# Kernel optimization log

Measured on AMD Instinct MI355X. Metric: run time of the kernel, lower is better.

Reference implementation:

```python
import jax, jax.numpy as jnp
import numpy as np

N, E, IN_F, H, F = 4096, 131072, 512, 8, 32  # n_nodes, n_edges, in_features, n_heads, n_hidden
SLOPE = 0.2


def setup_inputs() -> dict:
    key = jax.random.key(0)
    k1, k2, k3, k4 = jax.random.split(key, 4)
    h = jax.random.normal(k1, (N, IN_F), dtype=jnp.float32)
    edge_index = jax.random.randint(k2, (2, E), 0, N)
    train_mask = jnp.ones((E + N,), dtype=jnp.float32)  # mask values written into adj (incl. self-loops appended in forward)
    W_fc = jax.random.normal(k3, (IN_F, H * F), dtype=jnp.float32) * (1.0 / np.sqrt(IN_F))
    W_attn = jax.random.normal(k4, (2 * F,), dtype=jnp.float32) * (1.0 / np.sqrt(2 * F))
    return {"h": h, "edge_index": edge_index, "train_mask": train_mask, "W_fc": W_fc, "W_attn": W_attn}


def reference(h, edge_index, train_mask, W_fc, W_attn):
    n = h.shape[0]
    g = (h @ W_fc).reshape(n, H, F)  # [n, H, F]
    # attn_fc(concat(g_i, g_j)) == g_i @ W_attn[:F] + g_j @ W_attn[F:]  (same math, no NxNx2F tensor)
    el = g @ W_attn[:F]  # [n, H], contribution of source row i
    er = g @ W_attn[F:]  # [n, H], contribution of column j
    e = jax.nn.leaky_relu(el[:, None, :] + er[None, :, :], SLOPE)  # [n, n, H]
    # adjacency: edges (+ self-loops appended in forward) get train_mask values, then diagonal forced to 1
    src = jnp.concatenate([edge_index[0], jnp.arange(n)])
    dst = jnp.concatenate([edge_index[1], jnp.arange(n)])
    adj = jnp.zeros((n, n), dtype=h.dtype).at[src, dst].set(train_mask)
    diag = jnp.arange(n)
    adj = adj.at[diag, diag].set(1.0)
    e = jnp.where(adj[:, :, None] == 0, -jnp.inf, e)
    a = jax.nn.softmax(e, axis=1)  # softmax over neighbors j (dropout p=0 -> identity)
    attn_res = jnp.einsum('ijh,jhf->ihf', a, g)  # [n, H, F]
    return attn_res.reshape(n, H * F)  # is_concat=True
```

## Files before the change

kernel.cpp:

```cpp
#include <hip/hip_runtime.h>
#include <stdint.h>

#define NN   4096
#define NE   131072
#define KIN  512
#define NH   8
#define HF   256
#define SLOPE 0.2f
#define MAXJ 256

typedef __attribute__((ext_vector_type(8))) short bf16x8;
typedef __attribute__((ext_vector_type(4))) float f32x4;


__device__ __forceinline__ unsigned short f2bf(float x) {
  unsigned u = __builtin_bit_cast(unsigned, x);
  u += 0x7FFFu + ((u >> 16) & 1u);
  return (unsigned short)(u >> 16);
}
__device__ __forceinline__ float bf2f(unsigned short x) {
  unsigned u = ((unsigned)x) << 16;
  return __builtin_bit_cast(float, u);
}
__device__ __forceinline__ unsigned pack2(float lo, float hi) {
  return (unsigned)f2bf(lo) | ((unsigned)f2bf(hi) << 16);
}

__global__ __launch_bounds__(256) void prep_k(const float* __restrict__ B,
                                              unsigned* __restrict__ bitmap,
                                              unsigned short* __restrict__ Btbf) {
  __shared__ float tile[32][33];
  const int b = blockIdx.x, t = threadIdx.x;
  if (b < 128) {
    float4* p = (float4*)bitmap + (size_t)b * 1024;
#pragma unroll
    for (int it = 0; it < 4; ++it)
      p[it * 256 + t] = make_float4(0.f, 0.f, 0.f, 0.f);
  } else {
    int bb = b - 128;
    int k0 = (bb >> 3) * 32, n0 = (bb & 7) * 32;
    int lr = t >> 3, lc = (t & 7) * 4;
    float4 v = *(const float4*)&B[(size_t)(k0 + lr) * HF + n0 + lc];
    tile[lr][lc] = v.x; tile[lr][lc + 1] = v.y; tile[lr][lc + 2] = v.z; tile[lr][lc + 3] = v.w;
    __syncthreads();
    ushort4 o;
    o.x = f2bf(tile[lc + 0][lr]); o.y = f2bf(tile[lc + 1][lr]);
    o.z = f2bf(tile[lc + 2][lr]); o.w = f2bf(tile[lc + 3][lr]);
    *(ushort4*)&Btbf[(size_t)(n0 + lr) * KIN + k0 + lc] = o;
  }
}

__global__ __launch_bounds__(256) void gemm_adj_k(const float* __restrict__ h,
                                                  const unsigned short* __restrict__ Bt,
                                                  const float* __restrict__ Wa,
                                                  unsigned short* __restrict__ gbf,
                                                  float* __restrict__ el,
                                                  float* __restrict__ er,
                                                  const int* __restrict__ ei,
                                                  const float* __restrict__ mask,
                                                  unsigned* __restrict__ bitmap) {
  __shared__ unsigned short smem[2][6144];
  const int bx = blockIdx.x, t = threadIdx.x;
  if (bx >= 512) {
    int k = (bx - 512) * 256 + t;
    int s, d; float m;
    if (k < NE) { s = ei[k]; d = ei[NE + k]; m = mask[k]; }
    else        { s = k - NE; d = s; m = 1.0f; }
    if (m != 0.0f) atomicOr(&bitmap[s * 128 + (d >> 5)], 1u << (d & 31));
    return;
  }
  const int gx = bx & 127, gy = bx >> 7;
  const int row0 = gx * 32, col0 = gy * 64;
  const int w = t >> 6, l = t & 63;
  const int wr = w >> 1, wc = w & 1;

  const int srow = t >> 3;
  const int sc   = l & 7;
  const int aoff = srow * 64 + (((t & 7) ^ (srow & 7)) << 3);
  const float* gA = &h[(size_t)(row0 + srow) * KIN + (t & 7) * 8];
  const int bsrow = (w << 3) + (l >> 3);
  const int schB  = sc ^ (bsrow & 7);
  const unsigned short* gB0 = &Bt[(size_t)(col0 + bsrow) * KIN + schB * 8];
  const unsigned short* gB1 = &Bt[(size_t)(col0 + 32 + bsrow) * KIN + schB * 8];

#define BSTAGE(bf, ks)                                                                            \
  do {                                                                                            \
    __builtin_amdgcn_global_load_lds(                                                             \
        (const __attribute__((address_space(1))) unsigned int*)(gB0 + (size_t)(ks) * 64),         \
        (__attribute__((address_space(3))) unsigned int*)(&smem[bf][2048 + w * 512]), 16, 0, 0);  \
    __builtin_amdgcn_global_load_lds(                                                             \
        (const __attribute__((address_space(1))) unsigned int*)(gB1 + (size_t)(ks) * 64),         \
        (__attribute__((address_space(3))) unsigned int*)(&smem[bf][4096 + w * 512]), 16, 0, 0);  \
  } while (0)

  f32x4 acc0 = {}, acc1 = {};
  {
    float4 va0 = *(const float4*)(gA);
    float4 va1 = *(const float4*)(gA + 4);
    BSTAGE(0, 0);
    uint4 w4 = {pack2(va0.x, va0.y), pack2(va0.z, va0.w),
                pack2(va1.x, va1.y), pack2(va1.z, va1.w)};
    *(uint4*)&smem[0][aoff] = w4;
  }
  __syncthreads();

  const int lrow = l & 15, kg = l >> 4;
  const int ar  = wr * 16 + lrow;
  const int br0 = wc * 32 + lrow, br1 = wc * 32 + 16 + lrow;
  for (int ks = 0; ks < 8; ++ks) {
    const int bf = ks & 1;
    float4 na0, na1;
    if (ks < 7) {
      na0 = *(const float4*)(gA + (ks + 1) * 64);
      na1 = *(const float4*)(gA + (ks + 1) * 64 + 4);
      BSTAGE(bf ^ 1, ks + 1);
    }
    bf16x8 a0 = *(const bf16x8*)&smem[bf][ar * 64 + ((kg ^ (ar & 7)) << 3)];
    bf16x8 a1 = *(const bf16x8*)&smem[bf][ar * 64 + (((4 + kg) ^ (ar & 7)) << 3)];
    bf16x8 b00 = *(const bf16x8*)&smem[bf][2048 + br0 * 64 + ((kg ^ (br0 & 7)) << 3)];
    bf16x8 b01 = *(const bf16x8*)&smem[bf][2048 + br0 * 64 + (((4 + kg) ^ (br0 & 7)) << 3)];
    bf16x8 b10 = *(const bf16x8*)&smem[bf][2048 + br1 * 64 + ((kg ^ (br1 & 7)) << 3)];
    bf16x8 b11 = *(const bf16x8*)&smem[bf][2048 + br1 * 64 + (((4 + kg) ^ (br1 & 7)) << 3)];
    acc0 = __builtin_amdgcn_mfma_f32_16x16x32_bf16(a0, b00, acc0, 0, 0, 0);
    acc0 = __builtin_amdgcn_mfma_f32_16x16x32_bf16(a1, b01, acc0, 0, 0, 0);
    acc1 = __builtin_amdgcn_mfma_f32_16x16x32_bf16(a0, b10, acc1, 0, 0, 0);
    acc1 = __builtin_amdgcn_mfma_f32_16x16x32_bf16(a1, b11, acc1, 0, 0, 0);
    if (ks < 7) {
      uint4 w4 = {pack2(na0.x, na0.y), pack2(na0.z, na0.w),
                  pack2(na1.x, na1.y), pack2(na1.z, na1.w)};
      *(uint4*)&smem[bf ^ 1][aoff] = w4;
    }
    __syncthreads();
  }
#undef BSTAGE

  const int crow = (l >> 4) * 4, ccol = l & 15;
  const int gr0 = row0 + wr * 16 + crow;
  const int gc0 = col0 + wc * 32 + ccol, gc1 = gc0 + 16;
#pragma unroll
  for (int q = 0; q < 4; ++q) {
    gbf[(size_t)(gr0 + q) * HF + gc0] = f2bf(acc0[q]);
    gbf[(size_t)(gr0 + q) * HF + gc1] = f2bf(acc1[q]);
  }

  const int head = (gy << 1) + wc;
  const float wal0 = Wa[ccol],      wal1 = Wa[16 + ccol];
  const float war0 = Wa[32 + ccol], war1 = Wa[48 + ccol];
#pragma unroll
  for (int q = 0; q < 4; ++q) {
    float pel = acc0[q] * wal0 + acc1[q] * wal1;
    float per = acc0[q] * war0 + acc1[q] * war1;
#pragma unroll
    for (int m = 8; m >= 1; m >>= 1) { pel += __shfl_xor(pel, m); per += __shfl_xor(per, m); }
    if (ccol == 0) {
      el[(gr0 + q) * NH + head] = pel;
      er[(gr0 + q) * NH + head] = per;
    }
  }
}

__global__ __launch_bounds__(512) void attn_k(const unsigned* __restrict__ bitmap,
                                              const unsigned short* __restrict__ gbf,
                                              const float* __restrict__ el_,
                                              const float* __restrict__ er_,
                                              float* __restrict__ out) {
  __shared__ unsigned short jl[8][MAXJ];
  const int t = threadIdx.x, wv = t >> 6, l = t & 63;
  const int i = blockIdx.x * 8 + wv;

  unsigned w0 = bitmap[i * 128 + l];
  unsigned w1 = bitmap[i * 128 + 64 + l];
  int cnt = __popc(w0) + __popc(w1);
  int incl = cnt;
#pragma unroll
  for (int d = 1; d < 64; d <<= 1) {
    int u = __shfl_up(incl, d);
    if (l >= d) incl += u;
  }
  int total = __shfl(incl, 63);
  if (total > MAXJ) total = MAXJ;
  int off = incl - cnt;
  unsigned short* J = jl[wv];
  while (w0) {
    int b = __ffs(w0) - 1;
    if (off < MAXJ) J[off] = (unsigned short)(l * 32 + b);
    ++off; w0 &= w0 - 1;
  }
  while (w1) {
    int b = __ffs(w1) - 1;
    if (off < MAXJ) J[off] = (unsigned short)((64 + l) * 32 + b);
    ++off; w1 &= w1 - 1;
  }
  __syncthreads();

  const int hh = l >> 3;
  const float elh = el_[i * NH + hh];
  const unsigned short* gp = gbf + (size_t)l * 4;
  f32x4 accA = {}, accB = {};
  float den0 = 0.f, den1 = 0.f;
  int k = 0;
  for (; k + 4 <= total; k += 4) {
    int j0 = J[k], j1 = J[k + 1], j2 = J[k + 2], j3 = J[k + 3];
    float e0 = elh + er_[j0 * NH + hh];
    float e1 = elh + er_[j1 * NH + hh];
    float e2 = elh + er_[j2 * NH + hh];
    float e3 = elh + er_[j3 * NH + hh];
    ushort4 g0 = *(const ushort4*)(gp + (size_t)j0 * HF);
    ushort4 g1 = *(const ushort4*)(gp + (size_t)j1 * HF);
    ushort4 g2 = *(const ushort4*)(gp + (size_t)j2 * HF);
    ushort4 g3 = *(const ushort4*)(gp + (size_t)j3 * HF);
    float l0 = e0 > 0.f ? e0 : SLOPE * e0;
    float l1 = e1 > 0.f ? e1 : SLOPE * e1;
    float l2 = e2 > 0.f ? e2 : SLOPE * e2;
    float l3 = e3 > 0.f ? e3 : SLOPE * e3;
    float wg0 = __expf(l0), wg1 = __expf(l1), wg2 = __expf(l2), wg3 = __expf(l3);
    den0 += wg0 + wg2; den1 += wg1 + wg3;
    accA[0] += wg0 * bf2f(g0.x); accB[0] += wg1 * bf2f(g1.x);
    accA[1] += wg0 * bf2f(g0.y); accB[1] += wg1 * bf2f(g1.y);
    accA[2] += wg0 * bf2f(g0.z); accB[2] += wg1 * bf2f(g1.z);
    accA[3] += wg0 * bf2f(g0.w); accB[3] += wg1 * bf2f(g1.w);
    accA[0] += wg2 * bf2f(g2.x); accB[0] += wg3 * bf2f(g3.x);
    accA[1] += wg2 * bf2f(g2.y); accB[1] += wg3 * bf2f(g3.y);
    accA[2] += wg2 * bf2f(g2.z); accB[2] += wg3 * bf2f(g3.z);
    accA[3] += wg2 * bf2f(g2.w); accB[3] += wg3 * bf2f(g3.w);
  }
  for (; k < total; ++k) {
    int j0 = J[k];
    float e0 = elh + er_[j0 * NH + hh];
    float l0 = e0 > 0.f ? e0 : SLOPE * e0;
    float wg0 = __expf(l0);
    ushort4 g0 = *(const ushort4*)(gp + (size_t)j0 * HF);
    den0 += wg0;
    accA[0] += wg0 * bf2f(g0.x); accA[1] += wg0 * bf2f(g0.y);
    accA[2] += wg0 * bf2f(g0.z); accA[3] += wg0 * bf2f(g0.w);
  }
  float inv = 1.f / (den0 + den1);
  float4 o = make_float4((accA[0] + accB[0]) * inv, (accA[1] + accB[1]) * inv,
                         (accA[2] + accB[2]) * inv, (accA[3] + accB[3]) * inv);
  *(float4*)&out[(size_t)i * HF + l * 4] = o;
}

extern "C" void kernel_launch(void* const* d_in, const int* in_sizes, int n_in,
                              void* d_out, int out_size, void* d_ws, size_t ws_size,
                              hipStream_t stream) {
  const float* h      = (const float*)d_in[0];
  const int*   ei     = (const int*)d_in[1];
  const float* mask   = (const float*)d_in[2];
  const float* W_fc   = (const float*)d_in[3];
  const float* W_attn = (const float*)d_in[4];
  float* out = (float*)d_out;

  char* ws = (char*)d_ws;
  unsigned* bitmap      = (unsigned*)ws;
  unsigned short* gbf   = (unsigned short*)(ws + (size_t)2 * 1024 * 1024);
  float* el             = (float*)(ws + (size_t)4 * 1024 * 1024);
  float* er             = (float*)(ws + (size_t)4 * 1024 * 1024 + 128 * 1024);
  unsigned short* Btbf  = (unsigned short*)(ws + (size_t)4 * 1024 * 1024 + 256 * 1024);

  prep_k<<<256, 256, 0, stream>>>(W_fc, bitmap, Btbf);
  gemm_adj_k<<<512 + 528, 256, 0, stream>>>(h, Btbf, W_attn, gbf, el, er, ei, mask, bitmap);
  attn_k<<<NN / 8, 512, 0, stream>>>(bitmap, gbf, el, er, out);
}
```

Measured before the change: 33.13 us.

## Enlarge GEMM tile to 64x64 per block and schedule adjacency blocks first

Each GEMM block now computes a 64x64 output tile instead of 32x64, with each wave holding four MFMA accumulators (2x2 sub-tiles). This halves the GEMM block count and reuses each staged A and B fragment across two MFMAs, cutting redundant loads of W_fc per output row. The bitmap-building blocks are moved to the low block indices so the atomic adjacency work is dispatched before the GEMM blocks. The costs are more registers and LDS per block and fewer GEMM blocks, which leaves less parallelism across the CUs.

```diff
diff --git a/kernel.cpp b/kernel.cpp
--- a/kernel.cpp
+++ b/kernel.cpp
@@ -59,88 +59,106 @@
                                                   const int* __restrict__ ei,
                                                   const float* __restrict__ mask,
                                                   unsigned* __restrict__ bitmap) {
-  __shared__ unsigned short smem[2][6144];
+  __shared__ unsigned short smem[2][8192];
   const int bx = blockIdx.x, t = threadIdx.x;
-  if (bx >= 512) {
-    int k = (bx - 512) * 256 + t;
+  if (bx < 528) {
+    int k = bx * 256 + t;
     int s, d; float m;
     if (k < NE) { s = ei[k]; d = ei[NE + k]; m = mask[k]; }
     else        { s = k - NE; d = s; m = 1.0f; }
     if (m != 0.0f) atomicOr(&bitmap[s * 128 + (d >> 5)], 1u << (d & 31));
     return;
   }
-  const int gx = bx & 127, gy = bx >> 7;
-  const int row0 = gx * 32, col0 = gy * 64;
+  const int g = bx - 528;
+  const int gx = g & 63, gy = g >> 6;
+  const int row0 = gx * 64, col0 = gy * 64;
   const int w = t >> 6, l = t & 63;
   const int wr = w >> 1, wc = w & 1;
 
-  const int srow = t >> 3;
-  const int sc   = l & 7;
-  const int aoff = srow * 64 + (((t & 7) ^ (srow & 7)) << 3);
-  const float* gA = &h[(size_t)(row0 + srow) * KIN + (t & 7) * 8];
-  const int bsrow = (w << 3) + (l >> 3);
-  const int schB  = sc ^ (bsrow & 7);
-  const unsigned short* gB0 = &Bt[(size_t)(col0 + bsrow) * KIN + schB * 8];
-  const unsigned short* gB1 = &Bt[(size_t)(col0 + 32 + bsrow) * KIN + schB * 8];
+  const int r0 = t >> 3, c0 = t & 7;
+  const int aoff0 = r0 * 64 + ((c0 ^ (r0 & 7)) << 3);
+  const int aoff1 = aoff0 + 2048;
+  const float* gA0 = &h[(size_t)(row0 + r0) * KIN + c0 * 8];
+  const float* gA1 = gA0 + 32 * KIN;
+  const int sch = (l & 7) ^ (l >> 3);
+  const unsigned short* gB0 = &Bt[(size_t)(col0 + (w << 3) + (l >> 3)) * KIN + sch * 8];
+  const unsigned short* gB1 = gB0 + 32 * KIN;
 
 #define BSTAGE(bf, ks)                                                                            \
   do {                                                                                            \
     __builtin_amdgcn_global_load_lds(                                                             \
         (const __attribute__((address_space(1))) unsigned int*)(gB0 + (size_t)(ks) * 64),         \
-        (__attribute__((address_space(3))) unsigned int*)(&smem[bf][2048 + w * 512]), 16, 0, 0);  \
+        (__attribute__((address_space(3))) unsigned int*)(&smem[bf][4096 + w * 512]), 16, 0, 0);  \
     __builtin_amdgcn_global_load_lds(                                                             \
         (const __attribute__((address_space(1))) unsigned int*)(gB1 + (size_t)(ks) * 64),         \
-        (__attribute__((address_space(3))) unsigned int*)(&smem[bf][4096 + w * 512]), 16, 0, 0);  \
+        (__attribute__((address_space(3))) unsigned int*)(&smem[bf][6144 + w * 512]), 16, 0, 0);  \
   } while (0)
 
-  f32x4 acc0 = {}, acc1 = {};
+  f32x4 acc00 = {}, acc01 = {}, acc10 = {}, acc11 = {};
   {
-    float4 va0 = *(const float4*)(gA);
-    float4 va1 = *(const float4*)(gA + 4);
+    float4 v00 = *(const float4*)(gA0), v01 = *(const float4*)(gA0 + 4);
+    float4 v10 = *(const float4*)(gA1), v11 = *(const float4*)(gA1 + 4);
     BSTAGE(0, 0);
-    uint4 w4 = {pack2(va0.x, va0.y), pack2(va0.z, va0.w),
-                pack2(va1.x, va1.y), pack2(va1.z, va1.w)};
-    *(uint4*)&smem[0][aoff] = w4;
+    uint4 w0 = {pack2(v00.x, v00.y), pack2(v00.z, v00.w),
+                pack2(v01.x, v01.y), pack2(v01.z, v01.w)};
+    uint4 w1 = {pack2(v10.x, v10.y), pack2(v10.z, v10.w),
+                pack2(v11.x, v11.y), pack2(v11.z, v11.w)};
+    *(uint4*)&smem[0][aoff0] = w0;
+    *(uint4*)&smem[0][aoff1] = w1;
   }
   __syncthreads();
 
   const int lrow = l & 15, kg = l >> 4;
-  const int ar  = wr * 16 + lrow;
-  const int br0 = wc * 32 + lrow, br1 = wc * 32 + 16 + lrow;
+  const int ar0 = wr * 32 + lrow, ar1 = ar0 + 16;
+  const int br0 = wc * 32 + lrow, br1 = br0 + 16;
   for (int ks = 0; ks < 8; ++ks) {
     const int bf = ks & 1;
-    float4 na0, na1;
+    float4 v00, v01, v10, v11;
     if (ks < 7) {
-      na0 = *(const float4*)(gA + (ks + 1) * 64);
-      na1 = *(const float4*)(gA + (ks + 1) * 64 + 4);
+      v00 = *(const float4*)(gA0 + (ks + 1) * 64);
+      v01 = *(const float4*)(gA0 + (ks + 1) * 64 + 4);
+      v10 = *(const float4*)(gA1 + (ks + 1) * 64);
+      v11 = *(const float4*)(gA1 + (ks + 1) * 64 + 4);
       BSTAGE(bf ^ 1, ks + 1);
     }
-    bf16x8 a0 = *(const bf16x8*)&smem[bf][ar * 64 + ((kg ^ (ar & 7)) << 3)];
-    bf16x8 a1 = *(const bf16x8*)&smem[bf][ar * 64 + (((4 + kg) ^ (ar & 7)) << 3)];
-    bf16x8 b00 = *(const bf16x8*)&smem[bf][2048 + br0 * 64 + ((kg ^ (br0 & 7)) << 3)];
-    bf16x8 b01 = *(const bf16x8*)&smem[bf][2048 + br0 * 64 + (((4 + kg) ^ (br0 & 7)) << 3)];
-    bf16x8 b10 = *(const bf16x8*)&smem[bf][2048 + br1 * 64 + ((kg ^ (br1 & 7)) << 3)];
-    bf16x8 b11 = *(const bf16x8*)&smem[bf][2048 + br1 * 64 + (((4 + kg) ^ (br1 & 7)) << 3)];
-    acc0 = __builtin_amdgcn_mfma_f32_16x16x32_bf16(a0, b00, acc0, 0, 0, 0);
-    acc0 = __builtin_amdgcn_mfma_f32_16x16x32_bf16(a1, b01, acc0, 0, 0, 0);
-    acc1 = __builtin_amdgcn_mfma_f32_16x16x32_bf16(a0, b10, acc1, 0, 0, 0);
-    acc1 = __builtin_amdgcn_mfma_f32_16x16x32_bf16(a1, b11, acc1, 0, 0, 0);
+    bf16x8 a00 = *(const bf16x8*)&smem[bf][ar0 * 64 + ((kg ^ (ar0 & 7)) << 3)];
+    bf16x8 a01 = *(const bf16x8*)&smem[bf][ar0 * 64 + (((4 + kg) ^ (ar0 & 7)) << 3)];
+    bf16x8 a10 = *(const bf16x8*)&smem[bf][ar1 * 64 + ((kg ^ (ar1 & 7)) << 3)];
+    bf16x8 a11 = *(const bf16x8*)&smem[bf][ar1 * 64 + (((4 + kg) ^ (ar1 & 7)) << 3)];
+    bf16x8 b00 = *(const bf16x8*)&smem[bf][4096 + br0 * 64 + ((kg ^ (br0 & 7)) << 3)];
+    bf16x8 b01 = *(const bf16x8*)&smem[bf][4096 + br0 * 64 + (((4 + kg) ^ (br0 & 7)) << 3)];
+    bf16x8 b10 = *(const bf16x8*)&smem[bf][4096 + br1 * 64 + ((kg ^ (br1 & 7)) << 3)];
+    bf16x8 b11 = *(const bf16x8*)&smem[bf][4096 + br1 * 64 + (((4 + kg) ^ (br1 & 7)) << 3)];
+    acc00 = __builtin_amdgcn_mfma_f32_16x16x32_bf16(a00, b00, acc00, 0, 0, 0);
+    acc00 = __builtin_amdgcn_mfma_f32_16x16x32_bf16(a01, b01, acc00, 0, 0, 0);
+    acc01 = __builtin_amdgcn_mfma_f32_16x16x32_bf16(a00, b10, acc01, 0, 0, 0);
+    acc01 = __builtin_amdgcn_mfma_f32_16x16x32_bf16(a01, b11, acc01, 0, 0, 0);
+    acc10 = __builtin_amdgcn_mfma_f32_16x16x32_bf16(a10, b00, acc10, 0, 0, 0);
+    acc10 = __builtin_amdgcn_mfma_f32_16x16x32_bf16(a11, b01, acc10, 0, 0, 0);
+    acc11 = __builtin_amdgcn_mfma_f32_16x16x32_bf16(a10, b10, acc11, 0, 0, 0);
+    acc11 = __builtin_amdgcn_mfma_f32_16x16x32_bf16(a11, b11, acc11, 0, 0, 0);
     if (ks < 7) {
-      uint4 w4 = {pack2(na0.x, na0.y), pack2(na0.z, na0.w),
-                  pack2(na1.x, na1.y), pack2(na1.z, na1.w)};
-      *(uint4*)&smem[bf ^ 1][aoff] = w4;
+      uint4 w0 = {pack2(v00.x, v00.y), pack2(v00.z, v00.w),
+                  pack2(v01.x, v01.y), pack2(v01.z, v01.w)};
+      uint4 w1 = {pack2(v10.x, v10.y), pack2(v10.z, v10.w),
+                  pack2(v11.x, v11.y), pack2(v11.z, v11.w)};
+      *(uint4*)&smem[bf ^ 1][aoff0] = w0;
+      *(uint4*)&smem[bf ^ 1][aoff1] = w1;
     }
     __syncthreads();
   }
 #undef BSTAGE
 
   const int crow = (l >> 4) * 4, ccol = l & 15;
-  const int gr0 = row0 + wr * 16 + crow;
-  const int gc0 = col0 + wc * 32 + ccol, gc1 = gc0 + 16;
 #pragma unroll
   for (int q = 0; q < 4; ++q) {
-    gbf[(size_t)(gr0 + q) * HF + gc0] = f2bf(acc0[q]);
-    gbf[(size_t)(gr0 + q) * HF + gc1] = f2bf(acc1[q]);
+    int grA = row0 + wr * 32 + crow + q;
+    int grB = grA + 16;
+    int gcA = col0 + wc * 32 + ccol;
+    gbf[(size_t)grA * HF + gcA]      = f2bf(acc00[q]);
+    gbf[(size_t)grA * HF + gcA + 16] = f2bf(acc01[q]);
+    gbf[(size_t)grB * HF + gcA]      = f2bf(acc10[q]);
+    gbf[(size_t)grB * HF + gcA + 16] = f2bf(acc11[q]);
   }
 
   const int head = (gy << 1) + wc;
@@ -148,13 +166,21 @@
   const float war0 = Wa[32 + ccol], war1 = Wa[48 + ccol];
 #pragma unroll
   for (int q = 0; q < 4; ++q) {
-    float pel = acc0[q] * wal0 + acc1[q] * wal1;
-    float per = acc0[q] * war0 + acc1[q] * war1;
-#pragma unroll
-    for (int m = 8; m >= 1; m >>= 1) { pel += __shfl_xor(pel, m); per += __shfl_xor(per, m); }
+    float pel0 = acc00[q] * wal0 + acc01[q] * wal1;
+    float per0 = acc00[q] * war0 + acc01[q] * war1;
+    float pel1 = acc10[q] * wal0 + acc11[q] * wal1;
+    float per1 = acc10[q] * war0 + acc11[q] * war1;
+#pragma unroll
+    for (int m = 8; m >= 1; m >>= 1) {
+      pel0 += __shfl_xor(pel0, m); per0 += __shfl_xor(per0, m);
+      pel1 += __shfl_xor(pel1, m); per1 += __shfl_xor(per1, m);
+    }
     if (ccol == 0) {
-      el[(gr0 + q) * NH + head] = pel;
-      er[(gr0 + q) * NH + head] = per;
+      int rA = row0 + wr * 32 + crow + q;
+      el[rA * NH + head] = pel0;
+      er[rA * NH + head] = per0;
+      el[(rA + 16) * NH + head] = pel1;
+      er[(rA + 16) * NH + head] = per1;
     }
   }
 }
@@ -258,6 +284,6 @@
   unsigned short* Btbf  = (unsigned short*)(ws + (size_t)4 * 1024 * 1024 + 256 * 1024);
 
   prep_k<<<256, 256, 0, stream>>>(W_fc, bitmap, Btbf);
-  gemm_adj_k<<<512 + 528, 256, 0, stream>>>(h, Btbf, W_attn, gbf, el, er, ei, mask, bitmap);
+  gemm_adj_k<<<528 + 256, 256, 0, stream>>>(h, Btbf, W_attn, gbf, el, er, ei, mask, bitmap);
   attn_k<<<NN / 8, 512, 0, stream>>>(bitmap, gbf, el, er, out);
 }
```

Result: slower. 34.33 us (+3.6%).
